# Optimization experiments

Measured on AMD Instinct MI355X. Metric: run time of the kernel, lower is better.

## Reference

```python
import jax, jax.numpy as jnp
import numpy as np

N = 131072          # total rows across all types
IN_C = 512          # in_channels
OUT_C = 512         # out_channels
NUM_TYPES = 8       # len(types)


def setup_inputs() -> dict:
    key = jax.random.key(0)
    k1, k2, k3, k4 = jax.random.split(key, 4)
    x = jax.random.normal(k1, (N, IN_C), dtype=jnp.float32)
    type_vec = jnp.sort(jax.random.randint(k2, (N,), 0, NUM_TYPES)).astype(jnp.int64)
    # HeteroLinear params: weight [num_types, in, out], bias [num_types, out]
    scale = 1.0 / np.sqrt(IN_C)
    weight = jax.random.normal(k3, (NUM_TYPES, IN_C, OUT_C), dtype=jnp.float32) * scale
    bias = jax.random.normal(k4, (NUM_TYPES, OUT_C), dtype=jnp.float32) * scale
    return {"x": x, "type_vec": type_vec, "weight": weight, "bias": bias}


def _grouped_linear(x, type_vec, weight, bias):
    """out[n] = x[n] @ weight[type_vec[n]] + bias[type_vec[n]].

    Computed as T masked dense GEMMs (T is small) to avoid gathering a
    [N, in, out] per-row weight tensor.
    """
    n, out_c = x.shape[0], weight.shape[2]

    def per_type(acc, t):
        mask = (type_vec == t).astype(x.dtype)[:, None]  # [N, 1]
        y = (x * mask) @ weight[t] + mask * bias[t]      # [N, out]
        return acc + y, None

    out, _ = jax.lax.scan(per_type,
                          jnp.zeros((n, out_c), dtype=x.dtype),
                          jnp.arange(weight.shape[0]))
    return out


def reference(x, type_vec, weight, bias):
    # Equivalent to ToHeteroLinear.fused_forward (and dict_forward after the
    # cat/repeat_interleave, since type_vec is sorted / is_sorted=True).
    return _grouped_linear(x, type_vec, weight, bias)
```

## Files before the change

kernel.cpp:

```cpp
#include <hip/hip_runtime.h>

#define NROWS 131072
#define KDIM 512
#define NDIM 512

using short8  = __attribute__((ext_vector_type(8))) short;
using float4v = __attribute__((ext_vector_type(4))) float;
using uint4v  = __attribute__((ext_vector_type(4))) unsigned int;

__device__ __forceinline__ unsigned pack_trunc(float a, float b) {
    unsigned ua = __builtin_bit_cast(unsigned, a);
    unsigned ub = __builtin_bit_cast(unsigned, b);
    return __builtin_amdgcn_perm(ub, ua, 0x07060302u);
}
__device__ __forceinline__ unsigned pack_round(float a, float b) {
    unsigned ua = __builtin_bit_cast(unsigned, a) + 0x8000u;
    unsigned ub = __builtin_bit_cast(unsigned, b) + 0x8000u;
    return __builtin_amdgcn_perm(ub, ua, 0x07060302u);
}

__device__ __forceinline__ void glds16(const void* g, void* l) {
    __builtin_amdgcn_global_load_lds(
        (__attribute__((address_space(1))) void*)g,
        (__attribute__((address_space(3))) void*)l, 16, 0, 0);
}

__global__ __launch_bounds__(256) void wconv_kernel(const float* __restrict__ w,
                                                    unsigned short* __restrict__ wt) {
    int b  = blockIdx.x;
    int ty = b >> 6;
    int ot = (b >> 3) & 7;
    int it = b & 7;
    __shared__ float tile[64][65];
    const float* wp = w + ((size_t)ty << 18);
    int tid = threadIdx.x;
    int cf = tid & 15, ir0 = tid >> 4;
    #pragma unroll
    for (int j = 0; j < 4; ++j) {
        int ir = ir0 + 16 * j;
        float4v v = *(const float4v*)(wp + (size_t)(it * 64 + ir) * NDIM + ot * 64 + cf * 4);
        tile[ir][cf * 4 + 0] = v.x;
        tile[ir][cf * 4 + 1] = v.y;
        tile[ir][cf * 4 + 2] = v.z;
        tile[ir][cf * 4 + 3] = v.w;
    }
    __syncthreads();
    int oc = tid >> 2, iq = tid & 3;
    unsigned* op = (unsigned*)(wt + ((size_t)ty << 18) + (size_t)(ot * 64 + oc) * KDIM + it * 64 + iq * 16);
    #pragma unroll
    for (int j = 0; j < 8; ++j)
        op[j] = pack_round(tile[iq * 16 + 2 * j][oc], tile[iq * 16 + 2 * j + 1][oc]);
}

__global__ __launch_bounds__(256) void xconv_kernel(const float* __restrict__ x,
                                                    unsigned short* __restrict__ xb) {
    const size_t total = (size_t)NROWS * KDIM / 8;
    size_t i = (size_t)blockIdx.x * 256 + threadIdx.x;
    const size_t stride = (size_t)gridDim.x * 256;
    const float4v* xv = (const float4v*)x;
    uint4v* ov = (uint4v*)xb;
    for (; i < total; i += stride) {
        float4v a = __builtin_nontemporal_load(&xv[2 * i]);
        float4v c = __builtin_nontemporal_load(&xv[2 * i + 1]);
        uint4v o;
        o.x = pack_round(a.x, a.y);
        o.y = pack_round(a.z, a.w);
        o.z = pack_round(c.x, c.y);
        o.w = pack_round(c.z, c.w);
        ov[i] = o;
    }
}

__global__ __launch_bounds__(256, 3)
void hetero_gemm_pre(const unsigned short* __restrict__ xb,
                     const int* __restrict__ tv,
                     const unsigned short* __restrict__ wt,
                     const float* __restrict__ bias,
                     float* __restrict__ out) {
    __shared__ uint4v ldsA[2][4 * 128];
    __shared__ uint4v ldsB[2][4 * 128];

    const int b = blockIdx.x;
    const int rowTile = ((b >> 5) << 3) | (b & 7);
    const int colTile = (b >> 3) & 3;
    const int row0 = rowTile << 7;
    const int col0 = colTile << 7;

    const int tid  = threadIdx.x;
    const int lane = tid & 63;
    const int wave = tid >> 6;
    const int wm   = (wave & 1) << 6;
    const int wn   = (wave >> 1) << 6;
    const int l15  = lane & 15;
    const int quad = lane >> 4;

    const int i128 = tid & 127;
    const int g2   = tid >> 7;

    const int t0 = tv[row0];
    const int t1 = tv[row0 + 127];

    const unsigned short* abase = xb + (size_t)(row0 + i128) * KDIM + g2 * 8;

    for (int tt = t0; tt <= t1; ++tt) {
        const unsigned short* wbase =
            wt + ((size_t)tt << 18) + (size_t)(col0 + i128) * KDIM + g2 * 8;

        float4v acc[4][4];
        float4v zero = {0.f, 0.f, 0.f, 0.f};
        #pragma unroll
        for (int i = 0; i < 4; ++i)
            #pragma unroll
            for (int j = 0; j < 4; ++j)
                acc[i][j] = zero;

        glds16(abase,      &ldsA[0][ g2      * 128 + i128]);
        glds16(abase + 16, &ldsA[0][(g2 + 2) * 128 + i128]);
        glds16(wbase,      &ldsB[0][ g2      * 128 + i128]);
        glds16(wbase + 16, &ldsB[0][(g2 + 2) * 128 + i128]);
        __syncthreads();

        int cur = 0;
        for (int kc = 0; kc < KDIM; kc += 32) {
            if (kc + 32 < KDIM) {
                glds16(abase + kc + 32,      &ldsA[cur ^ 1][ g2      * 128 + i128]);
                glds16(abase + kc + 48,      &ldsA[cur ^ 1][(g2 + 2) * 128 + i128]);
                glds16(wbase + kc + 32,      &ldsB[cur ^ 1][ g2      * 128 + i128]);
                glds16(wbase + kc + 48,      &ldsB[cur ^ 1][(g2 + 2) * 128 + i128]);
            }

            short8 af[4], bf[4];
            #pragma unroll
            for (int mi = 0; mi < 4; ++mi)
                af[mi] = *(const short8*)&ldsA[cur][quad * 128 + wm + mi * 16 + l15];
            #pragma unroll
            for (int ni = 0; ni < 4; ++ni)
                bf[ni] = *(const short8*)&ldsB[cur][quad * 128 + wn + ni * 16 + l15];

            #pragma unroll
            for (int mi = 0; mi < 4; ++mi)
                #pragma unroll
                for (int ni = 0; ni < 4; ++ni)
                    acc[mi][ni] = __builtin_amdgcn_mfma_f32_16x16x32_bf16(
                        af[mi], bf[ni], acc[mi][ni], 0, 0, 0);

            __syncthreads();
            cur ^= 1;
        }

        float bcol[4];
        #pragma unroll
        for (int ni = 0; ni < 4; ++ni)
            bcol[ni] = bias[(size_t)tt * NDIM + col0 + wn + ni * 16 + l15];

        #pragma unroll
        for (int mi = 0; mi < 4; ++mi) {
            #pragma unroll
            for (int r = 0; r < 4; ++r) {
                const int grow = row0 + wm + mi * 16 + quad * 4 + r;
                if (tv[grow] == tt) {
                    float* orow = out + (size_t)grow * NDIM;
                    #pragma unroll
                    for (int ni = 0; ni < 4; ++ni) {
                        const int gcol = col0 + wn + ni * 16 + l15;
                        __builtin_nontemporal_store(acc[mi][ni][r] + bcol[ni], &orow[gcol]);
                    }
                }
            }
        }
    }
}

__global__ __launch_bounds__(256, 2)
void hetero_gemm_fallback(const float* __restrict__ x,
                          const int* __restrict__ tv,
                          const unsigned short* __restrict__ wt,
                          const float* __restrict__ bias,
                          float* __restrict__ out) {
    __shared__ uint4v ldsA[4 * 128];
    __shared__ uint4v ldsB[4 * 128];

    const int b = blockIdx.x;
    const int rowTile = ((b >> 5) << 3) | (b & 7);
    const int colTile = (b >> 3) & 3;
    const int row0 = rowTile << 7;
    const int col0 = colTile << 7;

    const int tid  = threadIdx.x;
    const int lane = tid & 63;
    const int wave = tid >> 6;
    const int wm   = (wave & 1) << 6;
    const int wn   = (wave >> 1) << 6;
    const int l15  = lane & 15;
    const int quad = lane >> 4;

    const int ra = tid >> 1;
    const int khalf = tid & 1;
    const int rtypeA = tv[row0 + ra];

    const int nb = tid & 127;
    const int g2 = tid >> 7;

    const int t0 = tv[row0];
    const int t1 = tv[row0 + 127];

    float4v acc[4][4];
    float4v zero = {0.f, 0.f, 0.f, 0.f};
    #pragma unroll
    for (int i = 0; i < 4; ++i)
        #pragma unroll
        for (int j = 0; j < 4; ++j)
            acc[i][j] = zero;

    for (int tt = t0; tt <= t1; ++tt) {
        const unsigned maskA = (rtypeA == tt) ? 0xFFFFFFFFu : 0u;
        const float* ap = x + (size_t)(row0 + ra) * KDIM + khalf * 16;
        const unsigned short* wb = wt + ((size_t)tt << 18) + (size_t)(col0 + nb) * KDIM;

        float4v av[4];
        uint4v  bv[2];
        #pragma unroll
        for (int i = 0; i < 4; ++i) av[i] = *(const float4v*)(ap + i * 4);
        bv[0] = *(const uint4v*)(wb + g2 * 8);
        bv[1] = *(const uint4v*)(wb + (g2 + 2) * 8);

        for (int kc = 0; kc < KDIM; kc += 32) {
            __syncthreads();
            uint4v pa0, pa1;
            pa0.x = pack_trunc(av[0].x, av[0].y) & maskA;
            pa0.y = pack_trunc(av[0].z, av[0].w) & maskA;
            pa0.z = pack_trunc(av[1].x, av[1].y) & maskA;
            pa0.w = pack_trunc(av[1].z, av[1].w) & maskA;
            pa1.x = pack_trunc(av[2].x, av[2].y) & maskA;
            pa1.y = pack_trunc(av[2].z, av[2].w) & maskA;
            pa1.z = pack_trunc(av[3].x, av[3].y) & maskA;
            pa1.w = pack_trunc(av[3].z, av[3].w) & maskA;
            ldsA[(khalf * 2 + 0) * 128 + ra] = pa0;
            ldsA[(khalf * 2 + 1) * 128 + ra] = pa1;
            ldsB[(g2    ) * 128 + nb] = bv[0];
            ldsB[(g2 + 2) * 128 + nb] = bv[1];
            __syncthreads();

            if (kc + 32 < KDIM) {
                const float* ap2 = ap + kc + 32;
                #pragma unroll
                for (int i = 0; i < 4; ++i) av[i] = *(const float4v*)(ap2 + i * 4);
                const unsigned short* wb2 = wb + kc + 32;
                bv[0] = *(const uint4v*)(wb2 + g2 * 8);
                bv[1] = *(const uint4v*)(wb2 + (g2 + 2) * 8);
            }

            short8 af[4], bf[4];
            #pragma unroll
            for (int mi = 0; mi < 4; ++mi)
                af[mi] = *(const short8*)&ldsA[quad * 128 + wm + mi * 16 + l15];
            #pragma unroll
            for (int ni = 0; ni < 4; ++ni)
                bf[ni] = *(const short8*)&ldsB[quad * 128 + wn + ni * 16 + l15];
            #pragma unroll
            for (int mi = 0; mi < 4; ++mi)
                #pragma unroll
                for (int ni = 0; ni < 4; ++ni)
                    acc[mi][ni] = __builtin_amdgcn_mfma_f32_16x16x32_bf16(
                        af[mi], bf[ni], acc[mi][ni], 0, 0, 0);
        }
    }

    #pragma unroll
    for (int mi = 0; mi < 4; ++mi) {
        #pragma unroll
        for (int r = 0; r < 4; ++r) {
            const int grow = row0 + wm + mi * 16 + quad * 4 + r;
            const int rt = tv[grow];
            const float* brow = bias + (size_t)rt * NDIM;
            float* orow = out + (size_t)grow * NDIM;
            #pragma unroll
            for (int ni = 0; ni < 4; ++ni) {
                const int gcol = col0 + wn + ni * 16 + l15;
                orow[gcol] = acc[mi][ni][r] + brow[gcol];
            }
        }
    }
}

extern "C" void kernel_launch(void* const* d_in, const int* in_sizes, int n_in,
                              void* d_out, int out_size, void* d_ws, size_t ws_size,
                              hipStream_t stream) {
    const float* x    = (const float*)d_in[0];
    const int*   tv   = (const int*)d_in[1];
    const float* w    = (const float*)d_in[2];
    const float* bias = (const float*)d_in[3];
    float* out = (float*)d_out;

    unsigned short* wtr = (unsigned short*)d_ws;
    const size_t WTN  = (size_t)8 * 512 * 512;
    const size_t NEED = WTN * 2 + (size_t)NROWS * KDIM * 2;

    wconv_kernel<<<512, 256, 0, stream>>>(w, wtr);
    if (ws_size >= NEED) {
        unsigned short* xb = wtr + WTN;
        xconv_kernel<<<2048, 256, 0, stream>>>(x, xb);
        hetero_gemm_pre<<<4096, 256, 0, stream>>>(xb, tv, wtr, bias, out);
    } else {
        hetero_gemm_fallback<<<4096, 256, 0, stream>>>(x, tv, wtr, bias, out);
    }
}
```

Measured before the change: 671.1 us.

## Merge conversion kernels and deepen GEMM LDS pipeline to four stages

Fuses the weight and activation bf16 conversion kernels into one launch with blockIdx-based dispatch, removing a kernel launch. The main GEMM moves from a double-buffered LDS pipeline with __syncthreads to a 4-buffer, 3-deep prefetch using explicit vmcnt waits and a single barrier per k-step, aiming to hide global load latency better. LDS use doubles, so launch bounds drop to 2 blocks/CU, which lowers occupancy. Output stores switch from nontemporal to normal stores.

```diff
diff --git a/kernel.cpp b/kernel.cpp
--- a/kernel.cpp
+++ b/kernel.cpp
@@ -25,60 +25,61 @@
         (__attribute__((address_space(3))) void*)l, 16, 0, 0);
 }
 
-__global__ __launch_bounds__(256) void wconv_kernel(const float* __restrict__ w,
-                                                    unsigned short* __restrict__ wt) {
-    int b  = blockIdx.x;
-    int ty = b >> 6;
-    int ot = (b >> 3) & 7;
-    int it = b & 7;
+__global__ __launch_bounds__(256) void prep_kernel(const float* __restrict__ w,
+                                                   unsigned short* __restrict__ wt,
+                                                   const float* __restrict__ x,
+                                                   unsigned short* __restrict__ xb) {
     __shared__ float tile[64][65];
-    const float* wp = w + ((size_t)ty << 18);
-    int tid = threadIdx.x;
-    int cf = tid & 15, ir0 = tid >> 4;
-    #pragma unroll
-    for (int j = 0; j < 4; ++j) {
-        int ir = ir0 + 16 * j;
-        float4v v = *(const float4v*)(wp + (size_t)(it * 64 + ir) * NDIM + ot * 64 + cf * 4);
-        tile[ir][cf * 4 + 0] = v.x;
-        tile[ir][cf * 4 + 1] = v.y;
-        tile[ir][cf * 4 + 2] = v.z;
-        tile[ir][cf * 4 + 3] = v.w;
-    }
-    __syncthreads();
-    int oc = tid >> 2, iq = tid & 3;
-    unsigned* op = (unsigned*)(wt + ((size_t)ty << 18) + (size_t)(ot * 64 + oc) * KDIM + it * 64 + iq * 16);
-    #pragma unroll
-    for (int j = 0; j < 8; ++j)
-        op[j] = pack_round(tile[iq * 16 + 2 * j][oc], tile[iq * 16 + 2 * j + 1][oc]);
-}
-
-__global__ __launch_bounds__(256) void xconv_kernel(const float* __restrict__ x,
-                                                    unsigned short* __restrict__ xb) {
-    const size_t total = (size_t)NROWS * KDIM / 8;
-    size_t i = (size_t)blockIdx.x * 256 + threadIdx.x;
-    const size_t stride = (size_t)gridDim.x * 256;
-    const float4v* xv = (const float4v*)x;
-    uint4v* ov = (uint4v*)xb;
-    for (; i < total; i += stride) {
-        float4v a = __builtin_nontemporal_load(&xv[2 * i]);
-        float4v c = __builtin_nontemporal_load(&xv[2 * i + 1]);
-        uint4v o;
-        o.x = pack_round(a.x, a.y);
-        o.y = pack_round(a.z, a.w);
-        o.z = pack_round(c.x, c.y);
-        o.w = pack_round(c.z, c.w);
-        ov[i] = o;
-    }
-}
-
-__global__ __launch_bounds__(256, 3)
+    if (blockIdx.x < 512) {
+        int b  = blockIdx.x;
+        int ty = b >> 6;
+        int ot = (b >> 3) & 7;
+        int it = b & 7;
+        const float* wp = w + ((size_t)ty << 18);
+        int tid = threadIdx.x;
+        int cf = tid & 15, ir0 = tid >> 4;
+        #pragma unroll
+        for (int j = 0; j < 4; ++j) {
+            int ir = ir0 + 16 * j;
+            float4v v = *(const float4v*)(wp + (size_t)(it * 64 + ir) * NDIM + ot * 64 + cf * 4);
+            tile[ir][cf * 4 + 0] = v.x;
+            tile[ir][cf * 4 + 1] = v.y;
+            tile[ir][cf * 4 + 2] = v.z;
+            tile[ir][cf * 4 + 3] = v.w;
+        }
+        __syncthreads();
+        int oc = tid >> 2, iq = tid & 3;
+        unsigned* op = (unsigned*)(wt + ((size_t)ty << 18) + (size_t)(ot * 64 + oc) * KDIM + it * 64 + iq * 16);
+        #pragma unroll
+        for (int j = 0; j < 8; ++j)
+            op[j] = pack_round(tile[iq * 16 + 2 * j][oc], tile[iq * 16 + 2 * j + 1][oc]);
+    } else {
+        const size_t total = (size_t)NROWS * KDIM / 8;
+        size_t i = (size_t)(blockIdx.x - 512) * 256 + threadIdx.x;
+        const size_t stride = (size_t)2048 * 256;
+        const float4v* xv = (const float4v*)x;
+        uint4v* ov = (uint4v*)xb;
+        for (; i < total; i += stride) {
+            float4v a = __builtin_nontemporal_load(&xv[2 * i]);
+            float4v c = __builtin_nontemporal_load(&xv[2 * i + 1]);
+            uint4v o;
+            o.x = pack_round(a.x, a.y);
+            o.y = pack_round(a.z, a.w);
+            o.z = pack_round(c.x, c.y);
+            o.w = pack_round(c.z, c.w);
+            ov[i] = o;
+        }
+    }
+}
+
+__global__ __launch_bounds__(256, 2)
 void hetero_gemm_pre(const unsigned short* __restrict__ xb,
                      const int* __restrict__ tv,
                      const unsigned short* __restrict__ wt,
                      const float* __restrict__ bias,
                      float* __restrict__ out) {
-    __shared__ uint4v ldsA[2][4 * 128];
-    __shared__ uint4v ldsB[2][4 * 128];
+    __shared__ uint4v ldsA[4][4 * 128];
+    __shared__ uint4v ldsB[4][4 * 128];
 
     const int b = blockIdx.x;
     const int rowTile = ((b >> 5) << 3) | (b & 7);
@@ -114,20 +115,28 @@
             for (int j = 0; j < 4; ++j)
                 acc[i][j] = zero;
 
-        glds16(abase,      &ldsA[0][ g2      * 128 + i128]);
-        glds16(abase + 16, &ldsA[0][(g2 + 2) * 128 + i128]);
-        glds16(wbase,      &ldsB[0][ g2      * 128 + i128]);
-        glds16(wbase + 16, &ldsB[0][(g2 + 2) * 128 + i128]);
-        __syncthreads();
-
-        int cur = 0;
-        for (int kc = 0; kc < KDIM; kc += 32) {
-            if (kc + 32 < KDIM) {
-                glds16(abase + kc + 32,      &ldsA[cur ^ 1][ g2      * 128 + i128]);
-                glds16(abase + kc + 48,      &ldsA[cur ^ 1][(g2 + 2) * 128 + i128]);
-                glds16(wbase + kc + 32,      &ldsB[cur ^ 1][ g2      * 128 + i128]);
-                glds16(wbase + kc + 48,      &ldsB[cur ^ 1][(g2 + 2) * 128 + i128]);
-            }
+#define STAGE(c, bufi)                                                       \
+    do {                                                                     \
+        glds16(abase + (c) * 32,      &ldsA[bufi][ g2      * 128 + i128]);   \
+        glds16(abase + (c) * 32 + 16, &ldsA[bufi][(g2 + 2) * 128 + i128]);   \
+        glds16(wbase + (c) * 32,      &ldsB[bufi][ g2      * 128 + i128]);   \
+        glds16(wbase + (c) * 32 + 16, &ldsB[bufi][(g2 + 2) * 128 + i128]);   \
+    } while (0)
+
+        STAGE(0, 0);
+        STAGE(1, 1);
+        STAGE(2, 2);
+
+        #pragma unroll
+        for (int k = 0; k < 16; ++k) {
+            if (k < 14)       asm volatile("s_waitcnt vmcnt(8)" ::: "memory");
+            else if (k == 14) asm volatile("s_waitcnt vmcnt(4)" ::: "memory");
+            else              asm volatile("s_waitcnt vmcnt(0)" ::: "memory");
+            __builtin_amdgcn_s_barrier();
+
+            const int cur = k & 3;
+
+            if (k + 3 < 16) STAGE(k + 3, (k + 3) & 3);
 
             short8 af[4], bf[4];
             #pragma unroll
@@ -143,10 +152,8 @@
                 for (int ni = 0; ni < 4; ++ni)
                     acc[mi][ni] = __builtin_amdgcn_mfma_f32_16x16x32_bf16(
                         af[mi], bf[ni], acc[mi][ni], 0, 0, 0);
-
-            __syncthreads();
-            cur ^= 1;
-        }
+        }
+#undef STAGE
 
         float bcol[4];
         #pragma unroll
@@ -163,7 +170,7 @@
                     #pragma unroll
                     for (int ni = 0; ni < 4; ++ni) {
                         const int gcol = col0 + wn + ni * 16 + l15;
-                        __builtin_nontemporal_store(acc[mi][ni][r] + bcol[ni], &orow[gcol]);
+                        orow[gcol] = acc[mi][ni][r] + bcol[ni];
                     }
                 }
             }
@@ -296,12 +303,12 @@
     const size_t WTN  = (size_t)8 * 512 * 512;
     const size_t NEED = WTN * 2 + (size_t)NROWS * KDIM * 2;
 
-    wconv_kernel<<<512, 256, 0, stream>>>(w, wtr);
     if (ws_size >= NEED) {
         unsigned short* xb = wtr + WTN;
-        xconv_kernel<<<2048, 256, 0, stream>>>(x, xb);
+        prep_kernel<<<2560, 256, 0, stream>>>(w, wtr, x, xb);
         hetero_gemm_pre<<<4096, 256, 0, stream>>>(xb, tv, wtr, bias, out);
     } else {
+        prep_kernel<<<512, 256, 0, stream>>>(w, wtr, x, nullptr);
         hetero_gemm_fallback<<<4096, 256, 0, stream>>>(x, tv, wtr, bias, out);
     }
 }
```

New measurement: 604.7 us. -9.9%, faster.
